# Kernel optimization log

Hardware: AMD Instinct MI355X
Metric: run time of the kernel (lower is better)

Reference implementation:

```python
import jax, jax.numpy as jnp
import numpy as np

B, T, C, H, HD = 2, 1024, 1024, 16, 64

def _l2norm(x):
    return x / jnp.maximum(jnp.linalg.norm(x, axis=-1, keepdims=True), 1e-12)

def _rms(x):
    return x * jax.lax.rsqrt(jnp.mean(x * x, axis=-1, keepdims=True) + 1e-6)

def _rope_tables(t, hd):
    inv = 1.0 / (10000.0 ** (jnp.arange(0, hd, 2, dtype=jnp.float32) / hd))
    fr = jnp.outer(jnp.arange(t, dtype=jnp.float32), inv)  # [T, hd/2]
    return jnp.cos(fr)[None, :, None, :], jnp.sin(fr)[None, :, None, :]

def _rope(x, cos, sin):
    h = x.shape[-1] // 2
    x1, x2 = x[..., :h], x[..., h:]
    return jnp.concatenate([x1 * cos + x2 * sin, -x1 * sin + x2 * cos], axis=-1)

def _qkv_heads(x, Wqkv, cos, sin):
    q, k, v = jnp.split(x @ Wqkv.T, 3, axis=-1)
    q = _rope(q.reshape(B, T, H, HD), cos, sin)
    k = _rope(k.reshape(B, T, H, HD), cos, sin)
    return q, k, v.reshape(B, T, H, HD)

def _bhtd(x):
    return jnp.swapaxes(x, 1, 2)

def _sdpa(q, k, v, scale, causal):
    s = jnp.einsum('bhqd,bhkd->bhqk', q, k) * scale
    s = jnp.where(causal, s, -jnp.inf)
    return jnp.einsum('bhqk,bhkd->bhqd', jax.nn.softmax(s, axis=-1), v)

def _hyp_attn(q, k, v, kc, causal):
    # project to Lorentz hyperboloid <x,x>_L = -k: time = sqrt(k + |x_s|^2)
    tq = jnp.sqrt(kc + jnp.sum(q * q, axis=-1, keepdims=True))  # [B,H,T,1]
    tk = jnp.sqrt(kc + jnp.sum(k * k, axis=-1, keepdims=True))
    # Lorentz inner product for all pairs, via GEMM (no [B,H,T,T,D+1] blowup)
    inner = jnp.einsum('bhqd,bhkd->bhqk', q, k) - tq * jnp.swapaxes(tk, -1, -2)
    # d(x,y) = sqrt(k) * arccosh(-<x,y>_L / k); clamp arg for numerical safety
    dist = jnp.sqrt(kc) * jnp.arccosh(jnp.maximum(-inner / kc, 1.0 + 1e-7))
    w = jnp.where(causal, 1.0 / (1e-6 + dist), -jnp.inf)
    return jnp.einsum('bhqk,bhkd->bhqd', jax.nn.softmax(w, axis=-1), v)

def _mlp(x, Wuv, Wmo, suv_eff=None):
    uv = x @ Wuv.T
    if suv_eff is not None:
        uv = suv_eff * uv
    u, v = jnp.split(uv, 2, axis=-1)
    return (u * jax.nn.silu(v)) @ Wmo.T

def _sph_skip(x, h, alpha):
    lr = jnp.abs(alpha * (0.05 * (C ** 0.5)))  # alpha * (init_value/init_scaling)
    a, b = _l2norm(x), _l2norm(h)
    return _l2norm(a + lr * (b - a))

def _euc_hyp_block(x, Wqkv, Wo, Wuv, Wmo, cos, sin, causal, kc=None):
    h = _rms(x)
    q, k, v = _qkv_heads(h, Wqkv, cos, sin)
    q, k, v = _bhtd(q), _bhtd(k), _bhtd(v)
    if kc is None:
        a = _sdpa(q, k, v, 1.0 / (C ** 0.5), causal)
    else:
        a = _hyp_attn(q, k, v, kc, causal)
    x = x + _bhtd(a).reshape(B, T, C) @ Wo.T
    x = x + _mlp(_rms(x), Wuv, Wmo)
    return x

def _sph_block(x, Wqkv, Wo, Wuv, Wmo, sqk, suv, attn_alpha, mlp_alpha, cos, sin, causal):
    q, k, v = _qkv_heads(x, Wqkv, cos, sin)
    sqk_eff = (sqk * (C ** 0.5)).reshape(1, 1, H, HD)  # sqk * init_value/init_scaling
    q = sqk_eff * _l2norm(q)
    k = sqk_eff * _l2norm(k)
    a = _sdpa(_bhtd(q), _bhtd(k), _bhtd(v), C ** 0.5, causal)
    x = _sph_skip(x, _bhtd(a).reshape(B, T, C) @ Wo.T, attn_alpha)
    x = _sph_skip(x, _mlp(x, Wuv, Wmo, suv_eff=suv * (C ** 0.5)), mlp_alpha)
    return x

def setup_inputs() -> dict:
    key = jax.random.key(0)
    ks = jax.random.split(key, 14)
    w = lambda k, shp: jax.random.normal(k, shp, jnp.float32) * 0.02
    inp = {'x': jax.random.normal(ks[0], (B, T, C), jnp.float32)}
    for i, g in enumerate(['euc', 'hyp', 'sph']):
        inp[f'Wqkv_{g}'] = w(ks[1 + 4 * i], (3 * C, C))
        inp[f'Wo_{g}'] = w(ks[2 + 4 * i], (C, C))
        inp[f'Wuv_{g}'] = w(ks[3 + 4 * i], (8 * C, C))
        inp[f'Wmo_{g}'] = w(ks[4 + 4 * i], (C, 4 * C))
    inp['k_hyp'] = jnp.ones((1, H, 1, 1), jnp.float32)
    inp['sqk'] = jnp.ones((C,), jnp.float32) / (C ** 0.5)
    inp['suv'] = jnp.ones((8 * C,), jnp.float32)
    inp['attn_alpha'] = jnp.ones((C,), jnp.float32) / (C ** 0.5)
    inp['mlp_alpha'] = jnp.ones((C,), jnp.float32) / (C ** 0.5)
    return inp

def reference(x, Wqkv_euc, Wo_euc, Wuv_euc, Wmo_euc,
              Wqkv_hyp, Wo_hyp, Wuv_hyp, Wmo_hyp, k_hyp,
              Wqkv_sph, Wo_sph, Wuv_sph, Wmo_sph,
              sqk, suv, attn_alpha, mlp_alpha):
    cos, sin = _rope_tables(T, HD)
    causal = jnp.tril(jnp.ones((T, T), dtype=bool))
    x = _euc_hyp_block(x, Wqkv_euc, Wo_euc, Wuv_euc, Wmo_euc, cos, sin, causal)
    x = _euc_hyp_block(x, Wqkv_hyp, Wo_hyp, Wuv_hyp, Wmo_hyp, cos, sin, causal, kc=k_hyp)
    x = _sph_block(x, Wqkv_sph, Wo_sph, Wuv_sph, Wmo_sph, sqk, suv, attn_alpha, mlp_alpha, cos, sin, causal)
    return x
```

## Files before the change

kernel.cpp:

```cpp
#include <hip/hip_runtime.h>
#include <stdint.h>
#include <stddef.h>

typedef __attribute__((ext_vector_type(8))) short short8;
typedef __attribute__((ext_vector_type(4))) float f32x4;
typedef unsigned short u16;
typedef unsigned int u32;

#define DEVI __device__ __forceinline__

static constexpr int T_ = 1024, C_ = 1024, M_ = 2048;

DEVI float bf2f(u16 u){ u32 x=((u32)u)<<16; float f; __builtin_memcpy(&f,&x,4); return f; }
DEVI u16 f2bf(float f){ u32 x; __builtin_memcpy(&x,&f,4); x += 0x7fffu + ((x>>16)&1u); return (u16)(x>>16); }

DEVI void gld_lds16(const u16* g, u16* l){
  __builtin_amdgcn_global_load_lds((const __attribute__((address_space(1))) void*)g,
                                   (__attribute__((address_space(3))) void*)l, 16, 0, 0);
}
DEVI f32x4 mfma16(short8 a, short8 b, f32x4 c){
  return __builtin_amdgcn_mfma_f32_16x16x32_bf16(a, b, c, 0, 0, 0);
}

__global__ void k_cast(const float* __restrict__ in, u16* __restrict__ out){
  int i = (blockIdx.x*blockDim.x + threadIdx.x)*4;
  float4 v = *(const float4*)(in+i);
  uint2 o; o.x = (u32)f2bf(v.x) | ((u32)f2bf(v.y)<<16);
  o.y = (u32)f2bf(v.z) | ((u32)f2bf(v.w)<<16);
  *(uint2*)(out+i) = o;
}

__global__ void k_tables(float* __restrict__ cosT, float* __restrict__ sinT){
  int i = blockIdx.x*256 + threadIdx.x;
  int t = i>>5, f = i&31;
  float inv = expf(-((float)f/32.f)*9.210340371976184f);
  float fr = (float)t * inv;
  cosT[i] = cosf(fr); sinT[i] = sinf(fr);
}

template<int NORM>
__global__ void k_rms(const float* __restrict__ x, u16* __restrict__ out){
  __shared__ float ps[4];
  int row = blockIdx.x, tid = threadIdx.x;
  float4 v = ((const float4*)(x + (size_t)row*C_))[tid];
  if (NORM){
    float ss = v.x*v.x+v.y*v.y+v.z*v.z+v.w*v.w;
    #pragma unroll
    for(int o=32;o>=1;o>>=1) ss += __shfl_xor(ss,o);
    if((tid&63)==0) ps[tid>>6]=ss;
    __syncthreads();
    ss = ps[0]+ps[1]+ps[2]+ps[3];
    float r = rsqrtf(ss*(1.f/C_) + 1e-6f);
    v.x*=r; v.y*=r; v.z*=r; v.w*=r;
  }
  uint2 o; o.x=(u32)f2bf(v.x)|((u32)f2bf(v.y)<<16);
  o.y=(u32)f2bf(v.z)|((u32)f2bf(v.w)<<16);
  ((uint2*)(out + (size_t)row*C_))[tid] = o;
}

template<int EPI>
__global__ __launch_bounds__(256) void k_gemm(const u16* __restrict__ A, const u16* __restrict__ Bw,
    void* __restrict__ Cout, const float* __restrict__ Res, int M, int N, int K){
  __shared__ u16 As[128*32];
  __shared__ u16 Bs[128*32];
  const int tid = threadIdx.x, w = tid>>6, lane = tid&63;
  const int bm = blockIdx.y<<7, bn = blockIdx.x<<7;
  const int wr = w>>1, wc = w&1;
  const int sr = lane>>2, sc = lane&3;
  f32x4 acc[4][4] = {};
  const u16* ga0 = A  + (size_t)(bm + w*32 + sr)*K + sc*8;
  const u16* gb0 = Bw + (size_t)(bn + w*32 + sr)*K + sc*8;
  u16* la0 = &As[(w*32)*32];
  u16* lb0 = &Bs[(w*32)*32];
  const int r16 = lane&15, ko = (lane>>4)*8;
  for (int k0=0; k0<K; k0+=32){
    __syncthreads();
    gld_lds16(ga0 + k0, la0);
    gld_lds16(ga0 + (size_t)16*K + k0, la0 + 16*32);
    gld_lds16(gb0 + k0, lb0);
    gld_lds16(gb0 + (size_t)16*K + k0, lb0 + 16*32);
    __syncthreads();
    short8 af[4], bf[4];
    #pragma unroll
    for(int mf=0;mf<4;++mf) af[mf] = *(const short8*)&As[(wr*64+mf*16+r16)*32 + ko];
    #pragma unroll
    for(int nf=0;nf<4;++nf) bf[nf] = *(const short8*)&Bs[(wc*64+nf*16+r16)*32 + ko];
    #pragma unroll
    for(int mf=0;mf<4;++mf)
      #pragma unroll
      for(int nf=0;nf<4;++nf)
        acc[mf][nf] = mfma16(af[mf], bf[nf], acc[mf][nf]);
  }
  const int rr = (lane>>4)*4;
  #pragma unroll
  for(int mf=0;mf<4;++mf){
    #pragma unroll
    for(int nf=0;nf<4;++nf){
      #pragma unroll
      for(int r=0;r<4;++r){
        size_t idx = (size_t)(bm + wr*64 + mf*16 + rr + r)*N + (bn + wc*64 + nf*16 + r16);
        float val = acc[mf][nf][r];
        if (EPI==0)      ((u16*)Cout)[idx] = f2bf(val);
        else if (EPI==1) ((float*)Cout)[idx] = Res[idx] + val;
        else             ((float*)Cout)[idx] = val;
      }
    }
  }
}

template<int SPH>
__global__ void k_ropeqk(const u16* __restrict__ qkv, const float* __restrict__ cosT,
                         const float* __restrict__ sinT, const float* __restrict__ sqk,
                         u16* __restrict__ Qb, u16* __restrict__ Kb){
  int idx = blockIdx.x*4 + (threadIdx.x>>6);
  int lane = threadIdx.x&63;
  int bh = idx>>10, t = idx&1023;
  int b = bh>>4, h = bh&15;
  size_t qa = (size_t)(b*T_ + t)*3072 + h*64 + lane;
  float qv = bf2f(qkv[qa]), kv = bf2f(qkv[qa + 1024]);
  float c = cosT[t*32 + (lane&31)], s = sinT[t*32 + (lane&31)];
  float qo = __shfl(qv, lane^32), ko2 = __shfl(kv, lane^32);
  float qr = (lane<32) ? (qv*c + qo*s) : (qv*c - qo*s);
  float kr = (lane<32) ? (kv*c + ko2*s) : (kv*c - ko2*s);
  if (SPH){
    float sq = qr*qr, sk = kr*kr;
    #pragma unroll
    for(int o=32;o>=1;o>>=1){ sq += __shfl_xor(sq,o); sk += __shfl_xor(sk,o); }
    float sc2 = sqk[h*64+lane]*32.f;
    qr = qr / fmaxf(sqrtf(sq),1e-12f) * sc2;
    kr = kr / fmaxf(sqrtf(sk),1e-12f) * sc2;
  }
  size_t oa = (size_t)bh*T_*64 + (size_t)t*64 + lane;
  Qb[oa] = f2bf(qr); Kb[oa] = f2bf(kr);
}

__global__ void k_vtrans(const u16* __restrict__ qkv, u16* __restrict__ Vt){
  __shared__ u16 tile[64][68];
  int bh = blockIdx.x, t0 = blockIdx.y*64;
  int b = bh>>4, h = bh&15;
  int tid = threadIdx.x;
  int tt = tid>>2, ch = tid&3;
  const u16* src = qkv + (size_t)(b*T_ + t0 + tt)*3072 + 2048 + h*64 + ch*16;
  short8 v0 = *(const short8*)src;
  short8 v1 = *(const short8*)(src+8);
  #pragma unroll
  for(int j=0;j<8;++j){ tile[tt][ch*16+j]=(u16)v0[j]; tile[tt][ch*16+8+j]=(u16)v1[j]; }
  __syncthreads();
  int d = tid>>2, tc = (tid&3)*16;
  short8 a, bb;
  #pragma unroll
  for(int j=0;j<8;++j){ a[j]=(short)tile[tc+j][d]; bb[j]=(short)tile[tc+8+j][d]; }
  u16* dst = Vt + ((size_t)bh*64 + d)*T_ + t0 + tc;
  *(short8*)dst = a; *(short8*)(dst+8) = bb;
}

template<int GEOM>
__global__ __launch_bounds__(64) void k_attn(const u16* __restrict__ Q, const u16* __restrict__ K,
    const u16* __restrict__ Vt, const float* __restrict__ khyp, u16* __restrict__ Oo){
  __shared__ u16 P[16*32];
  int qt = blockIdx.x, bh = blockIdx.y;
  int b = bh>>4, h = bh&15;
  int lane = threadIdx.x;
  int r16 = lane&15, g = lane>>4, ko = g*8;
  const u16* Qp = Q + (size_t)bh*T_*64;
  const u16* Kp = K + (size_t)bh*T_*64;
  const u16* Vp = Vt + (size_t)bh*64*T_;
  short8 qf0 = *(const short8*)&Qp[(size_t)(qt*16 + r16)*64 + ko];
  short8 qf1 = *(const short8*)&Qp[(size_t)(qt*16 + r16)*64 + 32 + ko];
  float kc=1.f, sqkc=1.f, tqr[4];
  if (GEOM==1){
    kc = khyp[h]; sqkc = sqrtf(kc);
    float ss=0;
    #pragma unroll
    for(int j=0;j<8;++j){ float a=bf2f((u16)qf0[j]); ss+=a*a; a=bf2f((u16)qf1[j]); ss+=a*a; }
    ss += __shfl_xor(ss,16); ss += __shfl_xor(ss,32);
    float tq = sqrtf(kc + ss);
    #pragma unroll
    for(int r=0;r<4;++r) tqr[r] = __shfl(tq, g*4+r);
  }
  f32x4 of[4] = {};
  float m[4], l[4];
  #pragma unroll
  for(int r=0;r<4;++r){ m[r]=-1e30f; l[r]=0.f; }
  int ntiles = (qt*16 + 16 + 31)>>5;
  for(int it=0; it<ntiles; ++it){
    int kt = it*32;
    short8 kf00 = *(const short8*)&Kp[(size_t)(kt + r16)*64 + ko];
    short8 kf01 = *(const short8*)&Kp[(size_t)(kt + r16)*64 + 32 + ko];
    short8 kf10 = *(const short8*)&Kp[(size_t)(kt + 16 + r16)*64 + ko];
    short8 kf11 = *(const short8*)&Kp[(size_t)(kt + 16 + r16)*64 + 32 + ko];
    f32x4 s0={}, s1={};
    s0 = mfma16(qf0, kf00, s0); s0 = mfma16(qf1, kf01, s0);
    s1 = mfma16(qf0, kf10, s1); s1 = mfma16(qf1, kf11, s1);
    float tk0=0.f, tk1=0.f;
    if (GEOM==1){
      float ss0=0, ss1=0;
      #pragma unroll
      for(int j=0;j<8;++j){
        float a=bf2f((u16)kf00[j]); ss0+=a*a; a=bf2f((u16)kf01[j]); ss0+=a*a;
        a=bf2f((u16)kf10[j]); ss1+=a*a; a=bf2f((u16)kf11[j]); ss1+=a*a;
      }
      ss0 += __shfl_xor(ss0,16); ss0 += __shfl_xor(ss0,32);
      ss1 += __shfl_xor(ss1,16); ss1 += __shfl_xor(ss1,32);
      tk0 = sqrtf(kc+ss0); tk1 = sqrtf(kc+ss1);
    }
    float w0[4], w1[4];
    #pragma unroll
    for(int r=0;r<4;++r){
      int qg = qt*16 + g*4 + r;
      float a0, a1;
      if (GEOM==0){ a0 = s0[r]*(1.f/32.f); a1 = s1[r]*(1.f/32.f); }
      else if (GEOM==2){ a0 = s0[r]*32.f; a1 = s1[r]*32.f; }
      else {
        float z0 = (tqr[r]*tk0 - s0[r])/kc; z0 = fmaxf(z0, 1.f+1e-7f);
        float z1 = (tqr[r]*tk1 - s1[r])/kc; z1 = fmaxf(z1, 1.f+1e-7f);
        float d0 = sqkc * logf(z0 + sqrtf(z0*z0 - 1.f));
        float d1 = sqkc * logf(z1 + sqrtf(z1*z1 - 1.f));
        a0 = 1.f/(1e-6f + d0); a1 = 1.f/(1e-6f + d1);
      }
      if (kt + r16 > qg)      a0 = -1e30f;
      if (kt + 16 + r16 > qg) a1 = -1e30f;
      w0[r]=a0; w1[r]=a1;
    }
    #pragma unroll
    for(int r=0;r<4;++r){
      float mt = fmaxf(w0[r], w1[r]);
      #pragma unroll
      for(int o=1;o<16;o<<=1) mt = fmaxf(mt, __shfl_xor(mt,o));
      float mn = fmaxf(m[r], mt);
      float alpha = __expf(m[r]-mn);
      m[r]=mn;
      float p0 = __expf(w0[r]-mn), p1 = __expf(w1[r]-mn);
      float rs = p0+p1;
      #pragma unroll
      for(int o=1;o<16;o<<=1) rs += __shfl_xor(rs,o);
      l[r] = l[r]*alpha + rs;
      #pragma unroll
      for(int vb=0;vb<4;++vb) of[vb][r] *= alpha;
      P[(g*4+r)*32 + r16]      = f2bf(p0);
      P[(g*4+r)*32 + 16 + r16] = f2bf(p1);
    }
    __syncthreads();
    short8 pf = *(const short8*)&P[r16*32 + ko];
    #pragma unroll
    for(int vb=0;vb<4;++vb){
      short8 vf = *(const short8*)&Vp[(size_t)(vb*16 + r16)*T_ + kt + ko];
      of[vb] = mfma16(pf, vf, of[vb]);
    }
    __syncthreads();
  }
  #pragma unroll
  for(int vb=0;vb<4;++vb){
    #pragma unroll
    for(int r=0;r<4;++r){
      int t = qt*16 + g*4 + r;
      Oo[((size_t)(b*T_ + t))*C_ + h*64 + vb*16 + r16] = f2bf(of[vb][r] / l[r]);
    }
  }
}

template<int SUV>
__global__ void k_silu(const u16* __restrict__ uv, const float* __restrict__ suv, u16* __restrict__ g){
  int i = blockIdx.x*256 + threadIdx.x;
  int m = i>>10, j = (i&1023)*4;
  const u16* up = uv + (size_t)m*8192 + j;
  uint2 uu = *(const uint2*)up;
  uint2 vv = *(const uint2*)(up+4096);
  float u[4] = { bf2f((u16)(uu.x&0xffff)), bf2f((u16)(uu.x>>16)), bf2f((u16)(uu.y&0xffff)), bf2f((u16)(uu.y>>16)) };
  float v[4] = { bf2f((u16)(vv.x&0xffff)), bf2f((u16)(vv.x>>16)), bf2f((u16)(vv.y&0xffff)), bf2f((u16)(vv.y>>16)) };
  float o[4];
  #pragma unroll
  for(int e=0;e<4;++e){
    float ue=u[e], ve=v[e];
    if (SUV){ ue *= suv[j+e]*32.0f; ve *= suv[4096+j+e]*32.0f; }
    o[e] = ue * (ve / (1.0f + __expf(-ve)));
  }
  uint2 oo; oo.x=(u32)f2bf(o[0])|((u32)f2bf(o[1])<<16); oo.y=(u32)f2bf(o[2])|((u32)f2bf(o[3])<<16);
  *(uint2*)(g + (size_t)m*4096 + j) = oo;
}

__global__ void k_sphskip(const float* __restrict__ x, const float* __restrict__ hh,
                          const float* __restrict__ alpha, float* __restrict__ out){
  __shared__ float red[3][4];
  int row = blockIdx.x, tid = threadIdx.x;
  float4 xv = ((const float4*)(x  + (size_t)row*C_))[tid];
  float4 hv = ((const float4*)(hh + (size_t)row*C_))[tid];
  float ssx = xv.x*xv.x+xv.y*xv.y+xv.z*xv.z+xv.w*xv.w;
  float ssh = hv.x*hv.x+hv.y*hv.y+hv.z*hv.z+hv.w*hv.w;
  #pragma unroll
  for(int o=32;o>=1;o>>=1){ ssx += __shfl_xor(ssx,o); ssh += __shfl_xor(ssh,o); }
  if((tid&63)==0){ red[0][tid>>6]=ssx; red[1][tid>>6]=ssh; }
  __syncthreads();
  ssx = red[0][0]+red[0][1]+red[0][2]+red[0][3];
  ssh = red[1][0]+red[1][1]+red[1][2]+red[1][3];
  float rx = 1.f/fmaxf(sqrtf(ssx),1e-12f), rh = 1.f/fmaxf(sqrtf(ssh),1e-12f);
  float4 al = ((const float4*)alpha)[tid];
  float y[4]; float ssy=0.f;
  { float a0=xv.x*rx, b0=hv.x*rh, lr=fabsf(al.x*1.6f); y[0]=a0+lr*(b0-a0); ssy+=y[0]*y[0]; }
  { float a0=xv.y*rx, b0=hv.y*rh, lr=fabsf(al.y*1.6f); y[1]=a0+lr*(b0-a0); ssy+=y[1]*y[1]; }
  { float a0=xv.z*rx, b0=hv.z*rh, lr=fabsf(al.z*1.6f); y[2]=a0+lr*(b0-a0); ssy+=y[2]*y[2]; }
  { float a0=xv.w*rx, b0=hv.w*rh, lr=fabsf(al.w*1.6f); y[3]=a0+lr*(b0-a0); ssy+=y[3]*y[3]; }
  #pragma unroll
  for(int o=32;o>=1;o>>=1) ssy += __shfl_xor(ssy,o);
  if((tid&63)==0) red[2][tid>>6]=ssy;
  __syncthreads();
  ssy = red[2][0]+red[2][1]+red[2][2]+red[2][3];
  float ry = 1.f/fmaxf(sqrtf(ssy),1e-12f);
  float4 o4; o4.x=y[0]*ry; o4.y=y[1]*ry; o4.z=y[2]*ry; o4.w=y[3]*ry;
  ((float4*)(out + (size_t)row*C_))[tid] = o4;
}

extern "C" void kernel_launch(void* const* d_in, const int* in_sizes, int n_in,
                              void* d_out, int out_size, void* d_ws, size_t ws_size,
                              hipStream_t stream){
  (void)n_in; (void)out_size; (void)ws_size;
  int i_khyp, sphb;
  if (in_sizes[9]==16){ i_khyp=9; sphb=10; } else { i_khyp=13; sphb=9; }
  const float* Wq[3] = {(const float*)d_in[1], (const float*)d_in[5], (const float*)d_in[sphb+0]};
  const float* Wo[3] = {(const float*)d_in[2], (const float*)d_in[6], (const float*)d_in[sphb+1]};
  const float* Wu[3] = {(const float*)d_in[3], (const float*)d_in[7], (const float*)d_in[sphb+2]};
  const float* Wm[3] = {(const float*)d_in[4], (const float*)d_in[8], (const float*)d_in[sphb+3]};
  const float* khyp = (const float*)d_in[i_khyp];
  const float* sqk  = (const float*)d_in[14];
  const float* suv  = (const float*)d_in[15];
  const float* aal  = (const float*)d_in[16];
  const float* mal  = (const float*)d_in[17];

  char* p = (char*)d_ws;
  auto alloc = [&](size_t bytes)->char*{ char* r=p; p += (bytes+255)&~(size_t)255; return r; };
  float* x    = (float*)alloc((size_t)M_*C_*4);
  float* hf32 = (float*)alloc((size_t)M_*C_*4);
  u16* h_bf   = (u16*)alloc((size_t)M_*C_*2);
  u16* qkv    = (u16*)alloc((size_t)M_*3072*2);
  u16* Qb     = (u16*)alloc((size_t)M_*1024*2);
  u16* Kb     = (u16*)alloc((size_t)M_*1024*2);
  u16* Vt     = (u16*)alloc((size_t)M_*1024*2);
  u16* att    = (u16*)alloc((size_t)M_*1024*2);
  u16* uvb    = (u16*)alloc((size_t)M_*8192*2);
  u16* gb     = (u16*)alloc((size_t)M_*4096*2);
  u16* wqb    = (u16*)alloc((size_t)3*C_*C_*2);
  u16* wob    = (u16*)alloc((size_t)C_*C_*2);
  u16* wub    = (u16*)alloc((size_t)8*C_*C_*2);
  u16* wmb    = (u16*)alloc((size_t)4*C_*C_*2);
  float* cosT = (float*)alloc((size_t)T_*32*4);
  float* sinT = (float*)alloc((size_t)T_*32*4);

  hipMemcpyAsync(x, d_in[0], (size_t)M_*C_*4, hipMemcpyDeviceToDevice, stream);
  k_tables<<<T_*32/256, 256, 0, stream>>>(cosT, sinT);

  for (int gi=0; gi<3; ++gi){
    bool sph = (gi==2);
    k_cast<<<3*C_*C_/1024, 256, 0, stream>>>(Wq[gi], wqb);
    k_cast<<<  C_*C_/1024, 256, 0, stream>>>(Wo[gi], wob);
    k_cast<<<8*C_*C_/1024, 256, 0, stream>>>(Wu[gi], wub);
    k_cast<<<4*C_*C_/1024, 256, 0, stream>>>(Wm[gi], wmb);

    if (!sph) k_rms<1><<<M_,256,0,stream>>>(x, h_bf);
    else      k_rms<0><<<M_,256,0,stream>>>(x, h_bf);
    k_gemm<0><<<dim3(24,16),256,0,stream>>>(h_bf, wqb, qkv, nullptr, M_, 3072, 1024);
    if (sph) k_ropeqk<1><<<8192,256,0,stream>>>(qkv, cosT, sinT, sqk, Qb, Kb);
    else     k_ropeqk<0><<<8192,256,0,stream>>>(qkv, cosT, sinT, nullptr, Qb, Kb);
    k_vtrans<<<dim3(32,16),256,0,stream>>>(qkv, Vt);
    if (gi==0)      k_attn<0><<<dim3(64,32),64,0,stream>>>(Qb,Kb,Vt,nullptr,att);
    else if (gi==1) k_attn<1><<<dim3(64,32),64,0,stream>>>(Qb,Kb,Vt,khyp,att);
    else            k_attn<2><<<dim3(64,32),64,0,stream>>>(Qb,Kb,Vt,nullptr,att);

    if (!sph){
      k_gemm<1><<<dim3(8,16),256,0,stream>>>(att, wob, x, x, M_, 1024, 1024);
      k_rms<1><<<M_,256,0,stream>>>(x, h_bf);
      k_gemm<0><<<dim3(64,16),256,0,stream>>>(h_bf, wub, uvb, nullptr, M_, 8192, 1024);
      k_silu<0><<<8192,256,0,stream>>>(uvb, nullptr, gb);
      k_gemm<1><<<dim3(8,16),256,0,stream>>>(gb, wmb, x, x, M_, 1024, 4096);
    } else {
      k_gemm<2><<<dim3(8,16),256,0,stream>>>(att, wob, hf32, nullptr, M_, 1024, 1024);
      k_sphskip<<<M_,256,0,stream>>>(x, hf32, aal, x);
      k_rms<0><<<M_,256,0,stream>>>(x, h_bf);
      k_gemm<0><<<dim3(64,16),256,0,stream>>>(h_bf, wub, uvb, nullptr, M_, 8192, 1024);
      k_silu<1><<<8192,256,0,stream>>>(uvb, suv, gb);
      k_gemm<2><<<dim3(8,16),256,0,stream>>>(gb, wmb, hf32, nullptr, M_, 1024, 4096);
      k_sphskip<<<M_,256,0,stream>>>(x, hf32, mal, (float*)d_out);
    }
  }
}
```

Before: 1.162 ms.

## Split attention along the key dimension and merge partials in a combine kernel

The attention kernel is split into chunks of 256 keys across a third grid dimension, so the long causal rows are spread over up to four workgroups. Each chunk writes unnormalised partial outputs plus its running max and sum in fp32. A new combine kernel rescales and sums these partials, then writes the bf16 output. This targets the load imbalance and low parallelism of the causal loop, at the cost of an extra launch and fp32 partial traffic stored in the reused uvb buffer.

```diff
diff --git a/kernel.cpp b/kernel.cpp
--- a/kernel.cpp
+++ b/kernel.cpp
@@ -155,10 +155,15 @@
 }
 
 template<int GEOM>
-__global__ __launch_bounds__(64) void k_attn(const u16* __restrict__ Q, const u16* __restrict__ K,
-    const u16* __restrict__ Vt, const float* __restrict__ khyp, u16* __restrict__ Oo){
+__global__ __launch_bounds__(64) void k_attn_split(const u16* __restrict__ Q, const u16* __restrict__ K,
+    const u16* __restrict__ Vt, const float* __restrict__ khyp,
+    float* __restrict__ partO, float* __restrict__ partML){
+  int qt = blockIdx.x, bh = blockIdx.y, ch = blockIdx.z;
+  int kend = qt*16 + 16;
+  int kbeg = ch*256;
+  if (kbeg >= kend) return;
+  int klim = min(kbeg + 256, kend);
   __shared__ u16 P[16*32];
-  int qt = blockIdx.x, bh = blockIdx.y;
   int b = bh>>4, h = bh&15;
   int lane = threadIdx.x;
   int r16 = lane&15, g = lane>>4, ko = g*8;
@@ -182,9 +187,9 @@
   float m[4], l[4];
   #pragma unroll
   for(int r=0;r<4;++r){ m[r]=-1e30f; l[r]=0.f; }
-  int ntiles = (qt*16 + 16 + 31)>>5;
+  int ntiles = (klim - kbeg + 31)>>5;
   for(int it=0; it<ntiles; ++it){
-    int kt = it*32;
+    int kt = kbeg + it*32;
     short8 kf00 = *(const short8*)&Kp[(size_t)(kt + r16)*64 + ko];
     short8 kf01 = *(const short8*)&Kp[(size_t)(kt + r16)*64 + 32 + ko];
     short8 kf10 = *(const short8*)&Kp[(size_t)(kt + 16 + r16)*64 + ko];
@@ -249,13 +254,52 @@
     }
     __syncthreads();
   }
-  #pragma unroll
-  for(int vb=0;vb<4;++vb){
+  size_t base = ((size_t)(bh*64 + qt)*4 + ch);
+  float* po = partO + base*1024;
+  #pragma unroll
+  for(int vb=0;vb<4;++vb)
+    #pragma unroll
+    for(int r=0;r<4;++r)
+      po[(g*4+r)*64 + vb*16 + r16] = of[vb][r];
+  if (r16 == 0){
     #pragma unroll
     for(int r=0;r<4;++r){
-      int t = qt*16 + g*4 + r;
-      Oo[((size_t)(b*T_ + t))*C_ + h*64 + vb*16 + r16] = f2bf(of[vb][r] / l[r]);
-    }
+      partML[(base*16 + g*4+r)*2    ] = m[r];
+      partML[(base*16 + g*4+r)*2 + 1] = l[r];
+    }
+  }
+}
+
+__global__ __launch_bounds__(64) void k_attn_combine(const float* __restrict__ partO,
+    const float* __restrict__ partML, u16* __restrict__ Oo){
+  int qt = blockIdx.x, bh = blockIdx.y;
+  int b = bh>>4, h = bh&15;
+  int lane = threadIdx.x;
+  int r16 = lane&15, g = lane>>4;
+  int nch = (qt>>4) + 1;
+  size_t base0 = ((size_t)(bh*64 + qt)*4);
+  #pragma unroll
+  for(int r=0;r<4;++r){
+    int row = g*4 + r;
+    float mstar = -1e30f;
+    for(int c=0;c<nch;++c)
+      mstar = fmaxf(mstar, partML[((base0+c)*16 + row)*2]);
+    float lstar = 0.f;
+    float ov[4] = {0.f,0.f,0.f,0.f};
+    for(int c=0;c<nch;++c){
+      float mc = partML[((base0+c)*16 + row)*2];
+      float lc = partML[((base0+c)*16 + row)*2 + 1];
+      float wgt = __expf(mc - mstar);
+      lstar += lc * wgt;
+      const float* po = partO + (base0+c)*1024 + row*64;
+      #pragma unroll
+      for(int vb=0;vb<4;++vb) ov[vb] += po[vb*16 + r16] * wgt;
+    }
+    float inv = 1.f / lstar;
+    int t = qt*16 + row;
+    #pragma unroll
+    for(int vb=0;vb<4;++vb)
+      Oo[((size_t)(b*T_ + t))*C_ + h*64 + vb*16 + r16] = f2bf(ov[vb] * inv);
   }
 }
 
@@ -344,6 +388,8 @@
   u16* wmb    = (u16*)alloc((size_t)4*C_*C_*2);
   float* cosT = (float*)alloc((size_t)T_*32*4);
   float* sinT = (float*)alloc((size_t)T_*32*4);
+  float* partO  = (float*)uvb;
+  float* partML = partO + (size_t)8*1024*1024;
 
   hipMemcpyAsync(x, d_in[0], (size_t)M_*C_*4, hipMemcpyDeviceToDevice, stream);
   k_tables<<<T_*32/256, 256, 0, stream>>>(cosT, sinT);
@@ -361,9 +407,10 @@
     if (sph) k_ropeqk<1><<<8192,256,0,stream>>>(qkv, cosT, sinT, sqk, Qb, Kb);
     else     k_ropeqk<0><<<8192,256,0,stream>>>(qkv, cosT, sinT, nullptr, Qb, Kb);
     k_vtrans<<<dim3(32,16),256,0,stream>>>(qkv, Vt);
-    if (gi==0)      k_attn<0><<<dim3(64,32),64,0,stream>>>(Qb,Kb,Vt,nullptr,att);
-    else if (gi==1) k_attn<1><<<dim3(64,32),64,0,stream>>>(Qb,Kb,Vt,khyp,att);
-    else            k_attn<2><<<dim3(64,32),64,0,stream>>>(Qb,Kb,Vt,nullptr,att);
+    if (gi==0)      k_attn_split<0><<<dim3(64,32,4),64,0,stream>>>(Qb,Kb,Vt,nullptr,partO,partML);
+    else if (gi==1) k_attn_split<1><<<dim3(64,32,4),64,0,stream>>>(Qb,Kb,Vt,khyp,partO,partML);
+    else            k_attn_split<2><<<dim3(64,32,4),64,0,stream>>>(Qb,Kb,Vt,nullptr,partO,partML);
+    k_attn_combine<<<dim3(64,32),64,0,stream>>>(partO, partML, att);
 
     if (!sph){
       k_gemm<1><<<dim3(8,16),256,0,stream>>>(att, wob, x, x, M_, 1024, 1024);
```

Result: faster. 1.124 ms (-3.3%).
